# Optimization experiments

Hardware: AMD Instinct MI355X
Metric: run time of the kernel (lower is better)

## Reference

```python
import jax, jax.numpy as jnp
import numpy as np

D_G, D_2D, D_3D = 512, 768, 1024
D_F, RANK, ATTN_H = 256, 16, 512
B = 8192


def _xavier(key, shape):
    fan_out, fan_in = shape
    lim = float(np.sqrt(6.0 / (fan_in + fan_out)))
    return jax.random.uniform(key, shape, jnp.float32, -lim, lim)


def setup_inputs() -> dict:
    key = jax.random.key(0)
    ks = jax.random.split(key, 12)
    inp = {
        "h_g": jax.random.normal(ks[0], (B, D_G), jnp.float32),
        "h_2d": jax.random.normal(ks[1], (B, D_2D), jnp.float32),
        "h_3d": jax.random.normal(ks[2], (B, D_3D), jnp.float32),
        # modality projections (torch Linear: y = x @ W.T + b)
        "Wg": _xavier(ks[3], (D_F, D_G)),   "bg": jnp.zeros((D_F,), jnp.float32),
        "W2": _xavier(ks[4], (D_F, D_2D)),  "b2": jnp.zeros((D_F,), jnp.float32),
        "W3": _xavier(ks[5], (D_F, D_3D)),  "b3": jnp.zeros((D_F,), jnp.float32),
        # LayerNorm affine params
        "ln_g_w": jnp.ones((D_F,), jnp.float32),  "ln_g_b": jnp.zeros((D_F,), jnp.float32),
        "ln_2_w": jnp.ones((D_F,), jnp.float32),  "ln_2_b": jnp.zeros((D_F,), jnp.float32),
        "ln_3_w": jnp.ones((D_F,), jnp.float32),  "ln_3_b": jnp.zeros((D_F,), jnp.float32),
        # rank expansions (no bias)
        "U": _xavier(ks[6], (RANK * D_F, D_F)),
        "V": _xavier(ks[7], (RANK * D_F, D_F)),
        "S": _xavier(ks[8], (RANK * D_F, D_F)),
        # attention MLP
        "Wa1": _xavier(ks[9], (ATTN_H, D_G + D_2D + D_3D)), "ba1": jnp.zeros((ATTN_H,), jnp.float32),
        "Wa2": _xavier(ks[10], (RANK, ATTN_H)),             "ba2": jnp.zeros((RANK,), jnp.float32),
    }
    return inp


def _layernorm(x, w, b, eps=1e-5):
    mu = jnp.mean(x, axis=-1, keepdims=True)
    var = jnp.var(x, axis=-1, keepdims=True)
    return (x - mu) * jax.lax.rsqrt(var + eps) * w + b


def reference(h_g, h_2d, h_3d, Wg, bg, W2, b2, W3, b3,
              ln_g_w, ln_g_b, ln_2_w, ln_2_b, ln_3_w, ln_3_b,
              U, V, S, Wa1, ba1, Wa2, ba2):
    # proj + LN + ReLU (dropout=0 / eval mode)
    g = jax.nn.relu(_layernorm(h_g @ Wg.T + bg, ln_g_w, ln_g_b))
    d2 = jax.nn.relu(_layernorm(h_2d @ W2.T + b2, ln_2_w, ln_2_b))
    d3 = jax.nn.relu(_layernorm(h_3d @ W3.T + b3, ln_3_w, ln_3_b))
    b = g.shape[0]
    # rank expansion: (B, R, d_f)
    g_r = (g @ U.T).reshape(b, RANK, D_F)
    d2_r = (d2 @ V.T).reshape(b, RANK, D_F)
    d3_r = (d3 @ S.T).reshape(b, RANK, D_F)
    z_r = g_r * d2_r * d3_r  # elementwise tri-linear product
    # rank attention from raw modality concat
    h_cat = jnp.concatenate([h_g, h_2d, h_3d], axis=-1)
    beta = jax.nn.softmax(jax.nn.relu(h_cat @ Wa1.T + ba1) @ Wa2.T + ba2, axis=-1)  # (B, R)
    z = jnp.einsum('brd,br->bd', z_r, beta)  # (B, d_f)
    return z
```

## Files before the change

### kernel.cpp

```cpp
#include <hip/hip_runtime.h>
#include <stdint.h>

#define B_ROWS 8192
#define DG 512
#define D2 768
#define D3 1024
#define DCAT 2304
#define DF 256
#define RANK 16
#define AH 512

#define OFF_WG 0
#define OFF_W2 131072
#define OFF_W3 327680
#define OFF_U  589824
#define OFF_V  1638400
#define OFF_S  2686976
#define OFF_WA1 3735552

#define WS_WBUF  0u
#define WS_HG    9830400u
#define WS_H2    18219008u
#define WS_H3    30801920u
#define WS_GBUF  9830400u
#define WS_PROJ  47579136u
#define WS_A1P   72744960u
#define WS_BETA  89522176u
#define WS_ZPART 47579136u
#define WS_REQUIRED 94240768u

typedef __attribute__((ext_vector_type(8))) short short8;
typedef __attribute__((ext_vector_type(4))) float f32x4;

__device__ inline unsigned short f2bf(float f) {
  union { float f; unsigned int u; } v; v.f = f;
  unsigned int u = v.u + 0x7fffu + ((v.u >> 16) & 1u);
  return (unsigned short)(u >> 16);
}
__device__ inline float bf2f(unsigned short h) {
  union { float f; unsigned int u; } v; v.u = ((unsigned int)h) << 16;
  return v.f;
}

typedef const unsigned int __attribute__((address_space(1)))* as1_u32p;
typedef unsigned int __attribute__((address_space(3)))* as3_u32p;

__device__ inline void g2l16(const unsigned short* g, unsigned short* l) {
  __builtin_amdgcn_global_load_lds((as1_u32p)g, (as3_u32p)l, 16, 0, 0);
}


__global__ __launch_bounds__(256) void cvt_split_k(const float* __restrict__ hg,
                                                   const float* __restrict__ h2,
                                                   const float* __restrict__ h3,
                                                   const float* __restrict__ Wg,
                                                   const float* __restrict__ W2,
                                                   const float* __restrict__ W3,
                                                   const float* __restrict__ U,
                                                   const float* __restrict__ V,
                                                   const float* __restrict__ S,
                                                   const float* __restrict__ Wa1,
                                                   unsigned short* __restrict__ hgb,
                                                   unsigned short* __restrict__ h2b,
                                                   unsigned short* __restrict__ h3b,
                                                   unsigned short* __restrict__ wbuf) {
  const int bid = blockIdx.x;
  const float* src;
  unsigned short* dst;
  int e;
  if (bid < 18432) {
    e = (bid * 256 + threadIdx.x) * 4;
    if (e < 4194304)        { src = hg + e;            dst = hgb + e; }
    else if (e < 10485760)  { src = h2 + (e - 4194304); dst = h2b + (e - 4194304); }
    else                    { src = h3 + (e - 10485760); dst = h3b + (e - 10485760); }
  } else {
    e = ((bid - 18432) * 256 + threadIdx.x) * 4;
    dst = wbuf + e;
    if (e < OFF_W2)       src = Wg  + e;
    else if (e < OFF_W3)  src = W2  + (e - OFF_W2);
    else if (e < OFF_U)   src = W3  + (e - OFF_W3);
    else if (e < OFF_V)   src = U   + (e - OFF_U);
    else if (e < OFF_S)   src = V   + (e - OFF_V);
    else if (e < OFF_WA1) src = S   + (e - OFF_S);
    else                  src = Wa1 + (e - OFF_WA1);
  }
  float4 v = *(const float4*)src;
  ushort4 o;
  o.x = f2bf(v.x); o.y = f2bf(v.y); o.z = f2bf(v.z); o.w = f2bf(v.w);
  *(ushort4*)dst = o;
}


__device__ __forceinline__ void gemm_mainloop_acc(const unsigned short* Ag, int lda,
                                                  const unsigned short* Bg, int ldb,
                                                  int K,
                                                  unsigned short* lA, unsigned short* lB,
                                                  f32x4 acc[4][4]) {
  const int tid = threadIdx.x;
  const int lane = tid & 63;
  const int wr = tid >> 7;
  const int wc = (tid >> 6) & 1;
  const int row_s = tid >> 3;
  const int kc_s = (((tid & 7) ^ ((tid >> 3) & 7)) << 3);
  const int mbase = wr * 64 + (lane & 15);
  const int nbase = wc * 64 + (lane & 15);
  const int kq = lane >> 4;
  const int h = lane & 7;

  const int nsteps = K >> 6;
  for (int ks = 0; ks < nsteps; ++ks) {
    const int k0 = ks << 6;
    __syncthreads();
#pragma unroll
    for (int p = 0; p < 4; ++p) {
      const int row = p * 32 + row_s;
      const int lofs = (p * 256 + tid) * 8;
      g2l16(Ag + (size_t)row * lda + k0 + kc_s, lA + lofs);
      g2l16(Bg + (size_t)row * ldb + k0 + kc_s, lB + lofs);
    }
    __syncthreads();
#pragma unroll
    for (int kk = 0; kk < 2; ++kk) {
      const int kch = (kk << 2) + kq;
      const int ko = ((kch ^ h) << 3);
      short8 af[4], bfr[4];
#pragma unroll
      for (int t = 0; t < 4; ++t) {
        af[t]  = *(const short8*)(lA + (mbase + t * 16) * 64 + ko);
        bfr[t] = *(const short8*)(lB + (nbase + t * 16) * 64 + ko);
      }
#pragma unroll
      for (int ti = 0; ti < 4; ++ti)
#pragma unroll
        for (int tj = 0; tj < 4; ++tj)
          acc[ti][tj] = __builtin_amdgcn_mfma_f32_16x16x32_bf16(af[ti], bfr[tj], acc[ti][tj], 0, 0, 0);
    }
  }
}

__device__ __forceinline__ void zero_acc(f32x4 acc[4][4]) {
#pragma unroll
  for (int i = 0; i < 4; ++i)
#pragma unroll
    for (int j = 0; j < 4; ++j)
      acc[i][j] = (f32x4){0.f, 0.f, 0.f, 0.f};
}


__global__ __launch_bounds__(256) void fatgemm_k(const unsigned short* __restrict__ hgb,
                                                 const unsigned short* __restrict__ h2b,
                                                 const unsigned short* __restrict__ h3b,
                                                 const unsigned short* __restrict__ wbuf,
                                                 float* __restrict__ proj,
                                                 unsigned short* __restrict__ a1part) {
  __shared__ __align__(16) unsigned short lA[128 * 64];
  __shared__ __align__(16) unsigned short lB[128 * 64];
  const int bid = blockIdx.x;
  f32x4 acc[4][4];
  const int lane = threadIdx.x & 63;
  const int wr = threadIdx.x >> 7, wc = (threadIdx.x >> 6) & 1;
  zero_acc(acc);

  if (bid < 512) {
    const int half = bid >> 8;
    const int local = bid & 255;
    const int m0 = (local >> 2) << 7;
    const int n0 = (local & 3) << 7;
    const unsigned short* Bb = wbuf + OFF_WA1 + (size_t)n0 * DCAT;
    if (half == 0) {
      gemm_mainloop_acc(hgb + (size_t)m0 * DG, DG, Bb, DCAT, DG, lA, lB, acc);
      gemm_mainloop_acc(h2b + (size_t)m0 * D2, D2, Bb + DG, DCAT, D2, lA, lB, acc);
    } else {
      gemm_mainloop_acc(h3b + (size_t)m0 * D3, D3, Bb + DG + D2, DCAT, D3, lA, lB, acc);
    }
    unsigned short* out = a1part + (size_t)half * (B_ROWS * AH);
    const int r0 = m0 + wr * 64 + ((lane >> 4) << 2);
    const int c0 = n0 + wc * 64 + (lane & 15);
#pragma unroll
    for (int ti = 0; ti < 4; ++ti)
#pragma unroll
      for (int tj = 0; tj < 4; ++tj)
#pragma unroll
        for (int i = 0; i < 4; ++i)
          out[(size_t)(r0 + ti * 16 + i) * AH + (c0 + tj * 16)] = f2bf(acc[ti][tj][i]);
  } else {
    const int b = bid - 512;
    const int z = b >> 7;
    const int local = b & 127;
    const int m0 = (local >> 1) << 7;
    const int n0 = (local & 1) << 7;
    const int Kz   = (z == 0) ? DG : (z == 1 ? D2 : D3);
    const unsigned short* Ab = (z == 0) ? hgb : (z == 1 ? h2b : h3b);
    const int woff = (z == 0) ? OFF_WG : (z == 1 ? OFF_W2 : OFF_W3);
    gemm_mainloop_acc(Ab + (size_t)m0 * Kz, Kz,
                      wbuf + woff + (size_t)n0 * Kz, Kz, Kz, lA, lB, acc);
    float* out = proj + (size_t)z * B_ROWS * DF;
    const int r0 = m0 + wr * 64 + ((lane >> 4) << 2);
    const int c0 = n0 + wc * 64 + (lane & 15);
#pragma unroll
    for (int ti = 0; ti < 4; ++ti)
#pragma unroll
      for (int tj = 0; tj < 4; ++tj)
#pragma unroll
        for (int i = 0; i < 4; ++i)
          out[(size_t)(r0 + ti * 16 + i) * DF + (c0 + tj * 16)] = acc[ti][tj][i];
  }
}


__global__ __launch_bounds__(256, 2) void rank_fused_k(const unsigned short* __restrict__ gbuf,
                                                       const unsigned short* __restrict__ wbuf,
                                                       const float* __restrict__ beta,
                                                       float* __restrict__ zpart) {
  __shared__ __align__(16) unsigned short lA[2 * 128 * 64];
  __shared__ __align__(16) unsigned short lB[2 * 128 * 64];
  __shared__ float lbeta[4 * 128];
  const int m0 = blockIdx.x * 128;
  const int d0 = blockIdx.y * 128;
  const int rg = blockIdx.z * 4;
  const int tid = threadIdx.x;

  for (int i = tid; i < 512; i += 256) {
    const int rr = i >> 7, row = i & 127;
    lbeta[i] = beta[(size_t)(m0 + row) * RANK + rg + rr];
  }
  __syncthreads();

  const int lane = tid & 63;
  const int wr = tid >> 7, wc = (tid >> 6) & 1;
  const int row_s = tid >> 3;
  const int kc_s = (((tid & 7) ^ ((tid >> 3) & 7)) << 3);
  const int mbase = wr * 64 + (lane & 15);
  const int nbase = wc * 64 + (lane & 15);
  const int kq = lane >> 4;
  const int h = lane & 7;
  const int lr0 = wr * 64 + ((lane >> 4) << 2);

  const unsigned short* Abase = gbuf + (size_t)(m0 + row_s) * DF + kc_s;
  const unsigned short* Bbase = wbuf + OFF_U + (size_t)(rg * 256 + d0 + row_s) * DF + kc_s;

  auto stage = [&](int t, unsigned short* dA, unsigned short* dB) {
    const int p = t >> 2, ks = t & 3;
    const int rr = p / 3;
    const int zi = p - rr * 3;
    const unsigned short* Ag = Abase + (size_t)zi * (B_ROWS * DF) + ks * 64;
    const unsigned short* Bg = Bbase + (size_t)zi * 1048576 + (size_t)rr * (256 * DF) + ks * 64;
#pragma unroll
    for (int q = 0; q < 4; ++q) {
      const int lofs = (q * 256 + tid) * 8;
      g2l16(Ag + (size_t)q * 32 * DF, dA + lofs);
      g2l16(Bg + (size_t)q * 32 * DF, dB + lofs);
    }
  };

  f32x4 zacc[4][4], prod[4][4], acc[4][4];
#pragma unroll
  for (int ti = 0; ti < 4; ++ti)
#pragma unroll
    for (int tj = 0; tj < 4; ++tj) {
      zacc[ti][tj] = (f32x4){0.f, 0.f, 0.f, 0.f};
      acc[ti][tj]  = (f32x4){0.f, 0.f, 0.f, 0.f};
    }

  auto compute = [&](const unsigned short* sA, const unsigned short* sB) {
#pragma unroll
    for (int kk = 0; kk < 2; ++kk) {
      const int kch = (kk << 2) + kq;
      const int ko = ((kch ^ h) << 3);
      short8 af[4], bfr[4];
#pragma unroll
      for (int t4 = 0; t4 < 4; ++t4) {
        af[t4]  = *(const short8*)(sA + (mbase + t4 * 16) * 64 + ko);
        bfr[t4] = *(const short8*)(sB + (nbase + t4 * 16) * 64 + ko);
      }
      __builtin_amdgcn_s_setprio(1);
#pragma unroll
      for (int ti = 0; ti < 4; ++ti)
#pragma unroll
        for (int tj = 0; tj < 4; ++tj)
          acc[ti][tj] = __builtin_amdgcn_mfma_f32_16x16x32_bf16(af[ti], bfr[tj], acc[ti][tj], 0, 0, 0);
      __builtin_amdgcn_s_setprio(0);
    }
  };

  stage(0, lA, lB);
  stage(1, lA + 8192, lB + 8192);

  for (int p = 0; p < 12; ++p) {
    const int rr = p / 3;
    const int zi = p - rr * 3;
#pragma unroll
    for (int ks = 0; ks < 4; ++ks) {
      const int t = (p << 2) + ks;
      const int b = t & 1;
      unsigned short* cA = lA + b * 8192;
      unsigned short* cB = lB + b * 8192;
      if (t < 47) asm volatile("s_waitcnt vmcnt(8)" ::: "memory");
      else        asm volatile("s_waitcnt vmcnt(0)" ::: "memory");
      __builtin_amdgcn_s_barrier();
      __builtin_amdgcn_sched_barrier(0);
      compute(cA, cB);
      __builtin_amdgcn_sched_barrier(0);
      __builtin_amdgcn_s_barrier();
      if (t + 2 < 48) stage(t + 2, cA, cB);
    }

    if (zi == 0) {
#pragma unroll
      for (int ti = 0; ti < 4; ++ti)
#pragma unroll
        for (int tj = 0; tj < 4; ++tj)
          prod[ti][tj] = acc[ti][tj];
    } else if (zi == 1) {
#pragma unroll
      for (int ti = 0; ti < 4; ++ti)
#pragma unroll
        for (int tj = 0; tj < 4; ++tj)
          prod[ti][tj] *= acc[ti][tj];
    } else {
#pragma unroll
      for (int ti = 0; ti < 4; ++ti) {
        const float4 b4 = *(const float4*)(lbeta + rr * 128 + lr0 + ti * 16);
        const float bv[4] = {b4.x, b4.y, b4.z, b4.w};
#pragma unroll
        for (int tj = 0; tj < 4; ++tj)
#pragma unroll
          for (int i = 0; i < 4; ++i)
            zacc[ti][tj][i] += prod[ti][tj][i] * acc[ti][tj][i] * bv[i];
      }
    }
#pragma unroll
    for (int ti = 0; ti < 4; ++ti)
#pragma unroll
      for (int tj = 0; tj < 4; ++tj)
        acc[ti][tj] = (f32x4){0.f, 0.f, 0.f, 0.f};
  }

  float* zp = zpart + (size_t)blockIdx.z * (B_ROWS * DF);
  const int c0 = d0 + wc * 64 + (lane & 15);
#pragma unroll
  for (int ti = 0; ti < 4; ++ti)
#pragma unroll
    for (int tj = 0; tj < 4; ++tj)
#pragma unroll
      for (int i = 0; i < 4; ++i)
        zp[(size_t)(m0 + lr0 + ti * 16 + i) * DF + (c0 + tj * 16)] = zacc[ti][tj][i];
}


__global__ __launch_bounds__(256) void zsum_k(const float* __restrict__ zpart,
                                              float* __restrict__ z) {
  const int idx = blockIdx.x * 256 + threadIdx.x;
  const size_t e = (size_t)idx * 4;
  const size_t stride = (size_t)B_ROWS * DF;
  float4 a = *(const float4*)(zpart + e);
  float4 b = *(const float4*)(zpart + stride + e);
  float4 c = *(const float4*)(zpart + 2 * stride + e);
  float4 d = *(const float4*)(zpart + 3 * stride + e);
  float4 o;
  o.x = (a.x + b.x) + (c.x + d.x);
  o.y = (a.y + b.y) + (c.y + d.y);
  o.z = (a.z + b.z) + (c.z + d.z);
  o.w = (a.w + b.w) + (c.w + d.w);
  *(float4*)(z + e) = o;
}


__global__ __launch_bounds__(256) void post_k(const float* __restrict__ proj,
                                              const float* __restrict__ bg, const float* __restrict__ b2, const float* __restrict__ b3,
                                              const float* __restrict__ wg, const float* __restrict__ wbg,
                                              const float* __restrict__ w2, const float* __restrict__ wb2,
                                              const float* __restrict__ w3, const float* __restrict__ wb3,
                                              unsigned short* __restrict__ gout,
                                              const unsigned short* __restrict__ a1part,
                                              const float* __restrict__ ba1,
                                              const float* __restrict__ Wa2,
                                              const float* __restrict__ ba2,
                                              float* __restrict__ beta) {
  const int bid = blockIdx.x;
  if (bid < 6144) {
    const int gid = bid * 4 + (threadIdx.x >> 6);
    const int lane = threadIdx.x & 63;
    const int z = gid >> 13;
    const int row = gid & (B_ROWS - 1);
    const float* bias = z == 0 ? bg : (z == 1 ? b2 : b3);
    const float* lw = z == 0 ? wg : (z == 1 ? w2 : w3);
    const float* lb = z == 0 ? wbg : (z == 1 ? wb2 : wb3);
    const float* x = proj + (size_t)z * B_ROWS * DF + (size_t)row * DF + lane * 4;
    float4 v = *(const float4*)x;
    float4 bb = *(const float4*)(bias + lane * 4);
    v.x += bb.x; v.y += bb.y; v.z += bb.z; v.w += bb.w;
    float s = v.x + v.y + v.z + v.w;
    float q = v.x * v.x + v.y * v.y + v.z * v.z + v.w * v.w;
#pragma unroll
    for (int m = 1; m < 64; m <<= 1) { s += __shfl_xor(s, m, 64); q += __shfl_xor(q, m, 64); }
    const float mean = s * (1.f / DF);
    const float var = q * (1.f / DF) - mean * mean;
    const float rs = rsqrtf(var + 1e-5f);
    float4 w4 = *(const float4*)(lw + lane * 4);
    float4 b4 = *(const float4*)(lb + lane * 4);
    ushort4 o;
    o.x = f2bf(fmaxf((v.x - mean) * rs * w4.x + b4.x, 0.f));
    o.y = f2bf(fmaxf((v.y - mean) * rs * w4.y + b4.y, 0.f));
    o.z = f2bf(fmaxf((v.z - mean) * rs * w4.z + b4.z, 0.f));
    o.w = f2bf(fmaxf((v.w - mean) * rs * w4.w + b4.w, 0.f));
    *(ushort4*)(gout + (size_t)z * B_ROWS * DF + (size_t)row * DF + lane * 4) = o;
  } else {
    __shared__ float lw[RANK * AH];
    for (int i = threadIdx.x; i < RANK * AH / 4; i += 256)
      *(float4*)(lw + i * 4) = *(const float4*)(Wa2 + i * 4);
    __syncthreads();
    const int row = (bid - 6144) * 4 + (threadIdx.x >> 6);
    const int lane = threadIdx.x & 63;
    const unsigned short* h0 = a1part + (size_t)row * AH + lane * 8;
    const unsigned short* h1 = h0 + (size_t)B_ROWS * AH;
    const uint4 p0 = *(const uint4*)h0;
    const uint4 p1 = *(const uint4*)h1;
    const unsigned int u0[4] = {p0.x, p0.y, p0.z, p0.w};
    const unsigned int u1[4] = {p1.x, p1.y, p1.z, p1.w};
    float4 ca = *(const float4*)(ba1 + lane * 8);
    float4 cb = *(const float4*)(ba1 + lane * 8 + 4);
    const float bias[8] = {ca.x, ca.y, ca.z, ca.w, cb.x, cb.y, cb.z, cb.w};
    float av[8];
#pragma unroll
    for (int j = 0; j < 4; ++j) {
      const float s0 = bf2f((unsigned short)(u0[j] & 0xffffu)) + bf2f((unsigned short)(u1[j] & 0xffffu));
      const float s1 = bf2f((unsigned short)(u0[j] >> 16)) + bf2f((unsigned short)(u1[j] >> 16));
      av[2 * j]     = fmaxf(s0 + bias[2 * j], 0.f);
      av[2 * j + 1] = fmaxf(s1 + bias[2 * j + 1], 0.f);
    }
    float lg[RANK];
#pragma unroll
    for (int r = 0; r < RANK; ++r) {
      const float* wrow = lw + r * AH + lane * 8;
      float4 wa = *(const float4*)wrow;
      float4 wb = *(const float4*)(wrow + 4);
      float p = av[0] * wa.x + av[1] * wa.y + av[2] * wa.z + av[3] * wa.w
              + av[4] * wb.x + av[5] * wb.y + av[6] * wb.z + av[7] * wb.w;
#pragma unroll
      for (int m = 1; m < 64; m <<= 1) p += __shfl_xor(p, m, 64);
      lg[r] = p + ba2[r];
    }
    float mx = lg[0];
#pragma unroll
    for (int r = 1; r < RANK; ++r) mx = fmaxf(mx, lg[r]);
    float den = 0.f;
#pragma unroll
    for (int r = 0; r < RANK; ++r) { lg[r] = __expf(lg[r] - mx); den += lg[r]; }
    const float inv = 1.f / den;
    if (lane < RANK) {
      float mine = 0.f;
#pragma unroll
      for (int r = 0; r < RANK; ++r) mine = (lane == r) ? lg[r] : mine;
      beta[(size_t)row * RANK + lane] = mine * inv;
    }
  }
}


extern "C" void kernel_launch(void* const* d_in, const int* in_sizes, int n_in,
                              void* d_out, int out_size, void* d_ws, size_t ws_size,
                              hipStream_t stream) {
  if (ws_size < (size_t)WS_REQUIRED) return;

  const float* h_g   = (const float*)d_in[0];
  const float* h_2d  = (const float*)d_in[1];
  const float* h_3d  = (const float*)d_in[2];
  const float* Wg    = (const float*)d_in[3];
  const float* bg    = (const float*)d_in[4];
  const float* W2    = (const float*)d_in[5];
  const float* b2    = (const float*)d_in[6];
  const float* W3    = (const float*)d_in[7];
  const float* b3    = (const float*)d_in[8];
  const float* ln_g_w = (const float*)d_in[9];
  const float* ln_g_b = (const float*)d_in[10];
  const float* ln_2_w = (const float*)d_in[11];
  const float* ln_2_b = (const float*)d_in[12];
  const float* ln_3_w = (const float*)d_in[13];
  const float* ln_3_b = (const float*)d_in[14];
  const float* U     = (const float*)d_in[15];
  const float* V     = (const float*)d_in[16];
  const float* S     = (const float*)d_in[17];
  const float* Wa1   = (const float*)d_in[18];
  const float* ba1   = (const float*)d_in[19];
  const float* Wa2   = (const float*)d_in[20];
  const float* ba2   = (const float*)d_in[21];

  char* ws = (char*)d_ws;
  unsigned short* wbuf   = (unsigned short*)(ws + WS_WBUF);
  unsigned short* hgb    = (unsigned short*)(ws + WS_HG);
  unsigned short* h2b    = (unsigned short*)(ws + WS_H2);
  unsigned short* h3b    = (unsigned short*)(ws + WS_H3);
  unsigned short* gbuf   = (unsigned short*)(ws + WS_GBUF);
  float*          proj   = (float*)(ws + WS_PROJ);
  unsigned short* a1part = (unsigned short*)(ws + WS_A1P);
  float*          beta   = (float*)(ws + WS_BETA);
  float*          zpart  = (float*)(ws + WS_ZPART);
  float* z = (float*)d_out;

  cvt_split_k<<<dim3(23232), dim3(256), 0, stream>>>(h_g, h_2d, h_3d,
                                                     Wg, W2, W3, U, V, S, Wa1,
                                                     hgb, h2b, h3b, wbuf);
  fatgemm_k<<<dim3(896), dim3(256), 0, stream>>>(hgb, h2b, h3b, wbuf, proj, a1part);
  post_k<<<dim3(8192), dim3(256), 0, stream>>>(proj, bg, b2, b3, ln_g_w, ln_g_b,
                                               ln_2_w, ln_2_b, ln_3_w, ln_3_b, gbuf,
                                               a1part, ba1, Wa2, ba2, beta);
  rank_fused_k<<<dim3(64, 2, 4), dim3(256), 0, stream>>>(gbuf, wbuf, beta, zpart);
  zsum_k<<<dim3(2048), dim3(256), 0, stream>>>(zpart, z);
}
```

Baseline: 303.4 us.

## Double-buffer LDS in fatgemm mainloop with async prefetch two tiles ahead

Replaces the single-buffered, two-barrier GEMM mainloop with a double-buffered pipeline. Global-to-LDS loads for tile t+2 are issued while tile t is computed, and a partial vmcnt wait keeps one stage in flight. MFMA blocks run at raised wave priority, and the attention GEMM's two K segments are merged into one continuous pipelined loop. LDS per block doubles to 64KB, which may limit occupancy despite the launch_bounds of 2 blocks per CU.

New measurement: 308.8 us. Within noise of the previous version (+1.8%).

```diff
diff --git a/kernel.cpp b/kernel.cpp
--- a/kernel.cpp
+++ b/kernel.cpp
@@ -90,75 +90,79 @@
   *(ushort4*)dst = o;
 }
 
-
-__device__ __forceinline__ void gemm_mainloop_acc(const unsigned short* Ag, int lda,
-                                                  const unsigned short* Bg, int ldb,
-                                                  int K,
-                                                  unsigned short* lA, unsigned short* lB,
-                                                  f32x4 acc[4][4]) {
+__device__ __forceinline__ void zero_acc(f32x4 acc[4][4]) {
+#pragma unroll
+  for (int i = 0; i < 4; ++i)
+#pragma unroll
+    for (int j = 0; j < 4; ++j)
+      acc[i][j] = (f32x4){0.f, 0.f, 0.f, 0.f};
+}
+
+
+template <typename F>
+__device__ __forceinline__ void pipe_run(int ntiles, F&& stage,
+                                         unsigned short* lA, unsigned short* lB,
+                                         f32x4 acc[4][4]) {
   const int tid = threadIdx.x;
   const int lane = tid & 63;
   const int wr = tid >> 7;
   const int wc = (tid >> 6) & 1;
-  const int row_s = tid >> 3;
-  const int kc_s = (((tid & 7) ^ ((tid >> 3) & 7)) << 3);
   const int mbase = wr * 64 + (lane & 15);
   const int nbase = wc * 64 + (lane & 15);
   const int kq = lane >> 4;
   const int h = lane & 7;
 
-  const int nsteps = K >> 6;
-  for (int ks = 0; ks < nsteps; ++ks) {
-    const int k0 = ks << 6;
-    __syncthreads();
-#pragma unroll
-    for (int p = 0; p < 4; ++p) {
-      const int row = p * 32 + row_s;
-      const int lofs = (p * 256 + tid) * 8;
-      g2l16(Ag + (size_t)row * lda + k0 + kc_s, lA + lofs);
-      g2l16(Bg + (size_t)row * ldb + k0 + kc_s, lB + lofs);
-    }
-    __syncthreads();
+  stage(0, lA, lB);
+  stage(1, lA + 8192, lB + 8192);
+
+  for (int t = 0; t < ntiles; ++t) {
+    const int b = t & 1;
+    unsigned short* cA = lA + b * 8192;
+    unsigned short* cB = lB + b * 8192;
+    if (t + 1 < ntiles) asm volatile("s_waitcnt vmcnt(8)" ::: "memory");
+    else               asm volatile("s_waitcnt vmcnt(0)" ::: "memory");
+    __builtin_amdgcn_s_barrier();
+    __builtin_amdgcn_sched_barrier(0);
 #pragma unroll
     for (int kk = 0; kk < 2; ++kk) {
       const int kch = (kk << 2) + kq;
       const int ko = ((kch ^ h) << 3);
       short8 af[4], bfr[4];
 #pragma unroll
-      for (int t = 0; t < 4; ++t) {
-        af[t]  = *(const short8*)(lA + (mbase + t * 16) * 64 + ko);
-        bfr[t] = *(const short8*)(lB + (nbase + t * 16) * 64 + ko);
+      for (int t4 = 0; t4 < 4; ++t4) {
+        af[t4]  = *(const short8*)(cA + (mbase + t4 * 16) * 64 + ko);
+        bfr[t4] = *(const short8*)(cB + (nbase + t4 * 16) * 64 + ko);
       }
+      __builtin_amdgcn_s_setprio(1);
 #pragma unroll
       for (int ti = 0; ti < 4; ++ti)
 #pragma unroll
         for (int tj = 0; tj < 4; ++tj)
           acc[ti][tj] = __builtin_amdgcn_mfma_f32_16x16x32_bf16(af[ti], bfr[tj], acc[ti][tj], 0, 0, 0);
-    }
+      __builtin_amdgcn_s_setprio(0);
+    }
+    __builtin_amdgcn_sched_barrier(0);
+    __builtin_amdgcn_s_barrier();
+    if (t + 2 < ntiles) stage(t + 2, cA, cB);
   }
 }
 
-__device__ __forceinline__ void zero_acc(f32x4 acc[4][4]) {
-#pragma unroll
-  for (int i = 0; i < 4; ++i)
-#pragma unroll
-    for (int j = 0; j < 4; ++j)
-      acc[i][j] = (f32x4){0.f, 0.f, 0.f, 0.f};
-}
-
-
-__global__ __launch_bounds__(256) void fatgemm_k(const unsigned short* __restrict__ hgb,
-                                                 const unsigned short* __restrict__ h2b,
-                                                 const unsigned short* __restrict__ h3b,
-                                                 const unsigned short* __restrict__ wbuf,
-                                                 float* __restrict__ proj,
-                                                 unsigned short* __restrict__ a1part) {
-  __shared__ __align__(16) unsigned short lA[128 * 64];
-  __shared__ __align__(16) unsigned short lB[128 * 64];
+
+__global__ __launch_bounds__(256, 2) void fatgemm_k(const unsigned short* __restrict__ hgb,
+                                                    const unsigned short* __restrict__ h2b,
+                                                    const unsigned short* __restrict__ h3b,
+                                                    const unsigned short* __restrict__ wbuf,
+                                                    float* __restrict__ proj,
+                                                    unsigned short* __restrict__ a1part) {
+  __shared__ __align__(16) unsigned short lA[2 * 128 * 64];
+  __shared__ __align__(16) unsigned short lB[2 * 128 * 64];
   const int bid = blockIdx.x;
+  const int tid = threadIdx.x;
   f32x4 acc[4][4];
-  const int lane = threadIdx.x & 63;
-  const int wr = threadIdx.x >> 7, wc = (threadIdx.x >> 6) & 1;
+  const int lane = tid & 63;
+  const int wr = tid >> 7, wc = (tid >> 6) & 1;
+  const int row_s = tid >> 3;
+  const int kc_s = (((tid & 7) ^ ((tid >> 3) & 7)) << 3);
   zero_acc(acc);
 
   if (bid < 512) {
@@ -167,12 +171,25 @@
     const int m0 = (local >> 2) << 7;
     const int n0 = (local & 3) << 7;
     const unsigned short* Bb = wbuf + OFF_WA1 + (size_t)n0 * DCAT;
-    if (half == 0) {
-      gemm_mainloop_acc(hgb + (size_t)m0 * DG, DG, Bb, DCAT, DG, lA, lB, acc);
-      gemm_mainloop_acc(h2b + (size_t)m0 * D2, D2, Bb + DG, DCAT, D2, lA, lB, acc);
-    } else {
-      gemm_mainloop_acc(h3b + (size_t)m0 * D3, D3, Bb + DG + D2, DCAT, D3, lA, lB, acc);
-    }
+    const int kwbase = (half == 0) ? 0 : (DG + D2);
+
+    auto stage_a1 = [&](int t, unsigned short* dA, unsigned short* dB) {
+      const unsigned short* Ag; int lda; int kb;
+      if (half == 0) {
+        if (t < 8) { Ag = hgb + (size_t)m0 * DG; lda = DG; kb = t * 64; }
+        else       { Ag = h2b + (size_t)m0 * D2; lda = D2; kb = (t - 8) * 64; }
+      } else       { Ag = h3b + (size_t)m0 * D3; lda = D3; kb = t * 64; }
+      const unsigned short* Bg = Bb + kwbase + t * 64;
+#pragma unroll
+      for (int p = 0; p < 4; ++p) {
+        const int row = p * 32 + row_s;
+        const int lofs = (p * 256 + tid) * 8;
+        g2l16(Ag + (size_t)row * lda + kb + kc_s, dA + lofs);
+        g2l16(Bg + (size_t)row * DCAT + kc_s, dB + lofs);
+      }
+    };
+    pipe_run((half == 0) ? 20 : 16, stage_a1, lA, lB, acc);
+
     unsigned short* out = a1part + (size_t)half * (B_ROWS * AH);
     const int r0 = m0 + wr * 64 + ((lane >> 4) << 2);
     const int c0 = n0 + wc * 64 + (lane & 15);
@@ -190,10 +207,22 @@
     const int m0 = (local >> 1) << 7;
     const int n0 = (local & 1) << 7;
     const int Kz   = (z == 0) ? DG : (z == 1 ? D2 : D3);
-    const unsigned short* Ab = (z == 0) ? hgb : (z == 1 ? h2b : h3b);
-    const int woff = (z == 0) ? OFF_WG : (z == 1 ? OFF_W2 : OFF_W3);
-    gemm_mainloop_acc(Ab + (size_t)m0 * Kz, Kz,
-                      wbuf + woff + (size_t)n0 * Kz, Kz, Kz, lA, lB, acc);
+    const unsigned short* Ab = ((z == 0) ? hgb : (z == 1 ? h2b : h3b)) + (size_t)m0 * Kz;
+    const unsigned short* Wb = wbuf + ((z == 0) ? OFF_WG : (z == 1 ? OFF_W2 : OFF_W3))
+                             + (size_t)n0 * Kz;
+
+    auto stage_pr = [&](int t, unsigned short* dA, unsigned short* dB) {
+      const int kb = t * 64;
+#pragma unroll
+      for (int p = 0; p < 4; ++p) {
+        const int row = p * 32 + row_s;
+        const int lofs = (p * 256 + tid) * 8;
+        g2l16(Ab + (size_t)row * Kz + kb + kc_s, dA + lofs);
+        g2l16(Wb + (size_t)row * Kz + kb + kc_s, dB + lofs);
+      }
+    };
+    pipe_run(Kz >> 6, stage_pr, lA, lB, acc);
+
     float* out = proj + (size_t)z * B_ROWS * DF;
     const int r0 = m0 + wr * 64 + ((lane >> 4) << 2);
     const int c0 = n0 + wc * 64 + (lane & 15);
```
